# Performance work log

Hardware: AMD Instinct MI355X
Metric: run time of the kernel (lower is better)

The kernel has to match this reference:

```python
import jax, jax.numpy as jnp
import numpy as np

B, S, D = 4, 2048, 1024
H, HD = 16, 64            # num heads, head dim (H*HD == D)
FF = 4096                  # llama intermediate size
EPS = 1e-6
THETA = 10000.0


def rms_norm(x, w):
    v = jnp.mean(jnp.square(x), axis=-1, keepdims=True)
    return x * jax.lax.rsqrt(v + EPS) * w


def apply_rope(x, pos):
    # x: [B,H,S,HD]; HF llama rotate_half convention
    inv = 1.0 / (THETA ** (jnp.arange(0, HD, 2, dtype=jnp.float32) / HD))  # [HD/2]
    ang = pos[:, None].astype(jnp.float32) * inv[None, :]                   # [S,HD/2]
    cos = jnp.concatenate([jnp.cos(ang), jnp.cos(ang)], -1)[None, None]     # [1,1,S,HD]
    sin = jnp.concatenate([jnp.sin(ang), jnp.sin(ang)], -1)[None, None]
    x1, x2 = jnp.split(x, 2, axis=-1)
    return x * cos + jnp.concatenate([-x2, x1], axis=-1) * sin


def setup_inputs() -> dict:
    key = jax.random.key(0)
    ks = jax.random.split(key, 12)
    p = lambda k, shp: (0.02 * jax.random.normal(k, shp, dtype=jnp.float32))
    return {
        "chunk_hidden_states": jax.random.normal(ks[0], (B, S, D), dtype=jnp.float32),
        "Wq": p(ks[1], (D, D)),
        "Wk": p(ks[2], (D, D)),
        "Wv": p(ks[3], (D, D)),
        "Wo": p(ks[4], (D, D)),
        "ln1_w": jnp.ones((D,), dtype=jnp.float32),
        "ln2_w": jnp.ones((D,), dtype=jnp.float32),
        "Wgate": p(ks[5], (FF, D)),
        "Wup": p(ks[6], (FF, D)),
        "Wdown": p(ks[7], (D, FF)),
        "W_out": p(ks[8], (1024, D)),
        "b_out": jnp.zeros((1024,), dtype=jnp.float32),
    }


def reference(chunk_hidden_states, Wq, Wk, Wv, Wo, ln1_w, ln2_w,
              Wgate, Wup, Wdown, W_out, b_out):
    x = chunk_hidden_states                      # [B,S,D]
    pos = jnp.arange(S)

    # --- self attention block ---
    h = rms_norm(x, ln1_w)
    q = (h @ Wq.T).reshape(B, S, H, HD).transpose(0, 2, 1, 3)  # [B,H,S,HD]
    k = (h @ Wk.T).reshape(B, S, H, HD).transpose(0, 2, 1, 3)
    v = (h @ Wv.T).reshape(B, S, H, HD).transpose(0, 2, 1, 3)
    q = apply_rope(q, pos)
    k = apply_rope(k, pos)
    # attention_mask is None when the layer is called directly -> full (non-causal) attention
    scores = jnp.einsum("bhqd,bhkd->bhqk", q, k) / jnp.sqrt(jnp.float32(HD))
    attn = jax.nn.softmax(scores, axis=-1)
    ctx = jnp.einsum("bhqk,bhkd->bhqd", attn, v)             # [B,H,S,HD]
    ctx = ctx.transpose(0, 2, 1, 3).reshape(B, S, D)
    x = x + ctx @ Wo.T

    # --- MLP block (SwiGLU) ---
    h2 = rms_norm(x, ln2_w)
    mlp = (jax.nn.silu(h2 @ Wgate.T) * (h2 @ Wup.T)) @ Wdown.T
    x = x + mlp

    # --- output head ---
    logits = x @ W_out.T + b_out                 # [B,S,1024]
    return logits.reshape(-1, 8, 1024)
```

## Files before the change

### kernel.cpp

```cpp
#include <hip/hip_runtime.h>

#define TB 4
#define TS 2048
#define TD 1024
#define TH 16
#define THD 64
#define TFF 4096
#define TTOK (TB*TS)

typedef unsigned int  uint32;
typedef unsigned short u16;
typedef short s8v __attribute__((ext_vector_type(8)));
typedef short s4bf __attribute__((ext_vector_type(4)));
typedef float f4v __attribute__((ext_vector_type(4)));

#define BF16_MAGIC 0x3f803f80u

__device__ __forceinline__ u16 f2bf(float f){
    uint32 u = __float_as_uint(f);
    u += 0x7fffu + ((u >> 16) & 1u);
    return (u16)(u >> 16);
}
__device__ __forceinline__ float bf2f(u16 h){
    return __uint_as_float(((uint32)h) << 16);
}
__device__ __forceinline__ void gload_lds16(const void* g, void* l){
    __builtin_amdgcn_global_load_lds(
        (const __attribute__((address_space(1))) unsigned int*)g,
        (__attribute__((address_space(3))) unsigned int*)l,
        16, 0, 0);
}
__device__ __forceinline__ void bar(){
    asm volatile("" ::: "memory");
    __builtin_amdgcn_s_barrier();
    asm volatile("" ::: "memory");
}
#define WAITVM(N) asm volatile("s_waitcnt vmcnt(" #N ")" ::: "memory")

struct CvtDesc { const void* src; void* dst; int n; int mode; };
struct CvtArgs { CvtDesc d[13]; };

__global__ __launch_bounds__(256)
void cvt_all(CvtArgs a, const uint32* __restrict__ flag){
    const bool isbf = (*flag == BF16_MAGIC);
    CvtDesc dd = a.d[blockIdx.y];
    if (dd.mode == 2){
        float* cosT = (float*)dd.dst;
        float* sinT = cosT + TS*32;
        for (int i = blockIdx.x*256 + threadIdx.x; i < dd.n; i += 256*gridDim.x){
            int s = i >> 5, f = i & 31;
            double inv = pow(10000.0, -(double)f/32.0);
            double ang = (double)s * inv;
            cosT[i] = (float)cos(ang);
            sinT[i] = (float)sin(ang);
        }
        return;
    }
    int n4 = dd.n >> 2;
    if (dd.mode == 1){
        float* dst = (float*)dd.dst;
        for (int i = blockIdx.x*256 + threadIdx.x; i < n4; i += 256*gridDim.x){
            float4 v;
            if (isbf){
                ushort4 u = ((const ushort4*)dd.src)[i];
                v = make_float4(bf2f(u.x), bf2f(u.y), bf2f(u.z), bf2f(u.w));
            } else v = ((const float4*)dd.src)[i];
            ((float4*)dst)[i] = v;
        }
        return;
    }
    for (int i = blockIdx.x*256 + threadIdx.x; i < n4; i += 256*gridDim.x){
        ushort4 o;
        if (isbf) o = ((const ushort4*)dd.src)[i];
        else {
            float4 v = ((const float4*)dd.src)[i];
            o.x=f2bf(v.x); o.y=f2bf(v.y); o.z=f2bf(v.z); o.w=f2bf(v.w);
        }
        size_t di = i;
        if (dd.mode >= 3){
            int row = i >> 8, c4 = i & 255;
            int drow = ((row >> 6) << 7) + (row & 63) + ((dd.mode == 4) ? 64 : 0);
            di = (size_t)drow*256 + c4;
        }
        ((ushort4*)dd.dst)[di] = o;
    }
}

__global__ __launch_bounds__(256)
void rmsnorm_k(const float* __restrict__ x, const float* __restrict__ w, u16* __restrict__ out){
    int row = blockIdx.x, tid = threadIdx.x;
    float4 xv = ((const float4*)(x + (size_t)row*TD))[tid];
    float s = xv.x*xv.x + xv.y*xv.y + xv.z*xv.z + xv.w*xv.w;
    #pragma unroll
    for (int off = 32; off > 0; off >>= 1) s += __shfl_xor(s, off);
    __shared__ float red[4];
    if ((tid & 63) == 0) red[tid >> 6] = s;
    __syncthreads();
    float tot = red[0]+red[1]+red[2]+red[3];
    float rs = rsqrtf(tot * (1.0f/TD) + 1e-6f);
    float4 wv = ((const float4*)w)[tid];
    ushort4 o;
    o.x = f2bf(xv.x*rs*wv.x); o.y = f2bf(xv.y*rs*wv.y);
    o.z = f2bf(xv.z*rs*wv.z); o.w = f2bf(xv.w*rs*wv.w);
    ((ushort4*)(out + (size_t)row*TD))[tid] = o;
}

enum { EPI_ADDF32 = 1, EPI_OUT = 3, EPI_QKVROPE = 4, EPI_ADDBF16 = 5, EPI_GATEUP = 6 };

template<int EPI>
__global__ __launch_bounds__(256)
void gemm_bt(const u16* __restrict__ A, int lda,
             const u16* __restrict__ W, int ldw,
             int K,
             void* __restrict__ outp, int ldo,
             const float* __restrict__ bias,
             const uint32* __restrict__ flag,
             u16* __restrict__ q_out, u16* __restrict__ k_out, u16* __restrict__ vt_out,
             const float* __restrict__ cosT, const float* __restrict__ sinT,
             const float* __restrict__ resid)
{
    __shared__ __align__(16) u16 SMEM[2*128*64];
    u16* As = SMEM;
    u16* Bs = SMEM + 128*64;
    const int tid  = threadIdx.x;
    const int wave = tid >> 6;
    const int lane = tid & 63;
    const int nbx = gridDim.x;
    const int lin = blockIdx.y * nbx + blockIdx.x;
    const int swz = (lin & 7) * ((nbx * gridDim.y) >> 3) + (lin >> 3);
    const int tm = (swz / nbx) * 128;
    const int tn = (swz % nbx) * 128;
    const int wm = (wave >> 1) * 64;
    const int wn = (wave &  1) * 64;

    f4v acc[4][4] = {};

    const int srow8 = lane >> 3;
    const int ch    = lane & 7;
    const int lrow  = lane & 15;
    const int lq    = lane >> 4;

    const u16* Ag = A + (size_t)(tm + wave*32 + srow8)*lda + ((ch ^ srow8) << 3);
    const u16* Wg = W + (size_t)(tn + wave*32 + srow8)*ldw + ((ch ^ srow8) << 3);

    for (int k0 = 0; k0 < K; k0 += 64){
        __syncthreads();
        #pragma unroll
        for (int i8 = 0; i8 < 4; i8++){
            gload_lds16(Ag + (size_t)(i8*8)*lda + k0, As + (wave*32 + i8*8)*64);
            gload_lds16(Wg + (size_t)(i8*8)*ldw + k0, Bs + (wave*32 + i8*8)*64);
        }
        __syncthreads();

        #pragma unroll
        for (int kk = 0; kk < 2; kk++){
            s8v a[4], b[4];
            #pragma unroll
            for (int i = 0; i < 4; i++){
                int row = wm + i*16 + lrow;
                a[i] = *(const s8v*)(As + row*64 + (((kk*4 + lq) ^ (lrow & 7)) << 3));
            }
            #pragma unroll
            for (int j = 0; j < 4; j++){
                int row = wn + j*16 + lrow;
                b[j] = *(const s8v*)(Bs + row*64 + (((kk*4 + lq) ^ (lrow & 7)) << 3));
            }
            #pragma unroll
            for (int i = 0; i < 4; i++)
                #pragma unroll
                for (int j = 0; j < 4; j++)
                    acc[i][j] = __builtin_amdgcn_mfma_f32_16x16x32_bf16(a[i], b[j], acc[i][j], 0, 0, 0);
        }
    }

    if constexpr (EPI == EPI_QKVROPE){
        const int ncol0 = tn + wn;
        if (ncol0 < 2048){
            u16* dst = (ncol0 < 1024) ? q_out : k_out;
            const int cbase = ncol0 & 1023;
            #pragma unroll
            for (int i = 0; i < 4; i++){
                #pragma unroll
                for (int r = 0; r < 4; r++){
                    int row = tm + wm + i*16 + lq*4 + r;
                    int s = row & (TS-1);
                    #pragma unroll
                    for (int j = 0; j < 2; j++){
                        int d = j*16 + lrow;
                        float c  = cosT[s*32 + d];
                        float sn = sinT[s*32 + d];
                        float x1 = acc[i][j][r], x2 = acc[i][j+2][r];
                        dst[(size_t)row*TD + cbase + d]      = f2bf(x1*c - x2*sn);
                        dst[(size_t)row*TD + cbase + d + 32] = f2bf(x2*c + x1*sn);
                    }
                }
            }
        } else {
            #pragma unroll
            for (int i = 0; i < 4; i++)
                #pragma unroll
                for (int j = 0; j < 4; j++)
                    #pragma unroll
                    for (int r = 0; r < 4; r++){
                        int row = tm + wm + i*16 + lq*4 + r;
                        int col = ncol0 - 2048 + j*16 + lrow;
                        int bb = row >> 11, s = row & (TS-1);
                        int hh = col >> 6, hd = col & 63;
                        vt_out[((size_t)(bb*TH + hh)*THD + hd)*TS + s] = f2bf(acc[i][j][r]);
                    }
        }
        return;
    }

    bool obf = false;
    if (EPI == EPI_OUT) obf = (*flag == BF16_MAGIC);
    #pragma unroll
    for (int i = 0; i < 4; i++){
        #pragma unroll
        for (int j = 0; j < 4; j++){
            #pragma unroll
            for (int r = 0; r < 4; r++){
                int row = tm + wm + i*16 + lq*4 + r;
                int col = tn + wn + j*16 + lrow;
                size_t idx = (size_t)row*ldo + col;
                float val = acc[i][j][r];
                if constexpr (EPI == EPI_ADDF32){
                    float* o = (float*)outp;
                    o[idx] += val;
                } else if constexpr (EPI == EPI_ADDBF16){
                    ((u16*)outp)[idx] = f2bf(resid[idx] + val);
                } else {
                    float v2 = val + bias[col];
                    if (obf) ((u16*)outp)[idx] = f2bf(v2);
                    else     ((float*)outp)[idx] = v2;
                }
            }
        }
    }
}

template<int EPI>
__global__ __launch_bounds__(512, 2)
void gemm256(const u16* __restrict__ A, int lda,
             const u16* __restrict__ W, int ldw,
             int K,
             void* __restrict__ outp, int ldo,
             const float* __restrict__ resid)
{
    __shared__ __align__(16) u16 SM[2][2*256*64];
    const int tid  = threadIdx.x;
    const int wave = tid >> 6;
    const int lane = tid & 63;
    const int wm = wave >> 2;
    const int wn = wave & 3;
    const int lrow = lane & 15;
    const int lq   = lane >> 4;
    const int srow8 = lane >> 3;
    const int ch    = lane & 7;

    const int nbx = gridDim.x;
    const int lin = blockIdx.y * nbx + blockIdx.x;
    const int swz = (lin & 7) * ((nbx * gridDim.y) >> 3) + (lin >> 3);
    const int tm = (swz / nbx) * 256;
    const int tn = (swz % nbx) * 256;

    const int NT = K >> 6;

    const u16* Ag = A + (size_t)(tm + wave*8 + srow8)*lda + ((ch ^ srow8) << 3);
    const u16* Wg = W + (size_t)(tn + wave*8 + srow8)*ldw + ((ch ^ srow8) << 3);

    f4v acc[2][4][2][2] = {};
    s8v a[2][4];
    s8v b[2][2][2];

    auto stageA = [&](int bufi, int g, int t){
        size_t k0 = (size_t)t * 64;
        #pragma unroll
        for (int r = 0; r < 2; r++)
            gload_lds16(Ag + (size_t)(g*128 + r*64)*lda + k0,
                        &SM[bufi][(g*128 + r*64 + wave*8)*64]);
    };
    auto stageB = [&](int bufi, int h, int t){
        size_t k0 = (size_t)t * 64;
        #pragma unroll
        for (int r = 0; r < 2; r++)
            gload_lds16(Wg + (size_t)(h*128 + r*64)*ldw + k0,
                        &SM[bufi][256*64 + (h*128 + r*64 + wave*8)*64]);
    };
    auto ldA = [&](int bufi, int g){
        #pragma unroll
        for (int kk = 0; kk < 2; kk++)
            #pragma unroll
            for (int i = 0; i < 4; i++){
                int row = g*128 + wm*64 + i*16 + lrow;
                a[kk][i] = *(const s8v*)(&SM[bufi][row*64 + (((kk*4 + lq) ^ (lrow & 7)) << 3)]);
            }
    };
    auto ldB = [&](int bufi, int h){
        #pragma unroll
        for (int kk = 0; kk < 2; kk++)
            #pragma unroll
            for (int j = 0; j < 2; j++){
                int row = h*128 + wn*32 + j*16 + lrow;
                b[h][kk][j] = *(const s8v*)(&SM[bufi][256*64 + row*64 + (((kk*4 + lq) ^ (lrow & 7)) << 3)]);
            }
    };
    auto mmac = [&](int g, int h){
        __builtin_amdgcn_s_setprio(1);
        #pragma unroll
        for (int kk = 0; kk < 2; kk++)
            #pragma unroll
            for (int i = 0; i < 4; i++)
                #pragma unroll
                for (int j = 0; j < 2; j++)
                    acc[g][i][h][j] = __builtin_amdgcn_mfma_f32_16x16x32_bf16(
                        a[kk][i], b[h][kk][j], acc[g][i][h][j], 0, 0, 0);
        __builtin_amdgcn_s_setprio(0);
    };

    stageA(0,0,0); stageB(0,0,0); stageB(0,1,0); stageA(0,1,0);
    stageA(1,0,1); stageB(1,0,1); stageB(1,1,1);
    WAITVM(6); bar();

    for (int t = 0; t < NT-2; t += 2){
        ldA(0,0); ldB(0,0);
        stageA(1,1,t+1);
        bar(); mmac(0,0); bar();
        ldB(0,1);
        stageA(0,0,t+2);
        bar(); mmac(0,1); bar();
        ldA(0,1);
        stageB(0,0,t+2);
        bar(); mmac(1,0); bar();
        stageB(0,1,t+2);
        WAITVM(6);
        bar(); mmac(1,1); bar();
        ldA(1,0); ldB(1,0);
        stageA(0,1,t+2);
        bar(); mmac(0,0); bar();
        ldB(1,1);
        stageA(1,0,t+3);
        bar(); mmac(0,1); bar();
        ldA(1,1);
        stageB(1,0,t+3);
        bar(); mmac(1,0); bar();
        stageB(1,1,t+3);
        WAITVM(6);
        bar(); mmac(1,1); bar();
    }
    {
        ldA(0,0); ldB(0,0);
        stageA(1,1,NT-1);
        bar(); mmac(0,0); bar();
        ldB(0,1);
        bar(); mmac(0,1); bar();
        ldA(0,1);
        bar(); mmac(1,0); bar();
        WAITVM(0);
        bar(); mmac(1,1); bar();
        ldA(1,0); ldB(1,0);
        bar(); mmac(0,0); bar();
        ldB(1,1);
        bar(); mmac(0,1); bar();
        ldA(1,1);
        bar(); mmac(1,0); bar();
        mmac(1,1);
    }

    if constexpr (EPI == EPI_GATEUP){
        bar();
        float* X = (float*)&SM[0][0];
        const int uw = wm*2 + (wn & 1);
        if (wn >= 2){
            #pragma unroll
            for (int g = 0; g < 2; g++)
            #pragma unroll
            for (int i = 0; i < 4; i++)
            #pragma unroll
            for (int h = 0; h < 2; h++)
            #pragma unroll
            for (int j = 0; j < 2; j++)
            #pragma unroll
            for (int r = 0; r < 4; r++)
                X[uw*8192 + (g*64 + i*16 + lq*4 + r)*64
                          + ((h*32 + j*16 + lrow) ^ (lq << 3))] = acc[g][i][h][j][r];
        }
        bar();
        if (wn < 2){
            u16* o = (u16*)outp;
            #pragma unroll
            for (int g = 0; g < 2; g++)
            #pragma unroll
            for (int i = 0; i < 4; i++)
            #pragma unroll
            for (int h = 0; h < 2; h++)
            #pragma unroll
            for (int j = 0; j < 2; j++)
            #pragma unroll
            for (int r = 0; r < 4; r++){
                float gv = acc[g][i][h][j][r];
                float uv = X[uw*8192 + (g*64 + i*16 + lq*4 + r)*64
                                     + ((h*32 + j*16 + lrow) ^ (lq << 3))];
                float mres = (gv / (1.0f + __expf(-gv))) * uv;
                int row = tm + g*128 + wm*64 + i*16 + lq*4 + r;
                int ff  = (tn >> 1) + h*64 + wn*32 + j*16 + lrow;
                o[(size_t)row*TFF + ff] = f2bf(mres);
            }
        }
        return;
    }

    if constexpr (EPI == EPI_ADDBF16){
        u16* o = (u16*)outp;
        #pragma unroll
        for (int g = 0; g < 2; g++)
        #pragma unroll
        for (int i = 0; i < 4; i++)
        #pragma unroll
        for (int h = 0; h < 2; h++)
        #pragma unroll
        for (int j = 0; j < 2; j++)
        #pragma unroll
        for (int r = 0; r < 4; r++){
            int row = tm + g*128 + wm*64 + i*16 + lq*4 + r;
            int col = tn + h*128 + wn*32 + j*16 + lrow;
            size_t idx = (size_t)row*ldo + col;
            o[idx] = f2bf(resid[idx] + acc[g][i][h][j][r]);
        }
        return;
    }
}

__global__ __launch_bounds__(256, 2)
void flash_attn_mfma(const u16* __restrict__ qg, const u16* __restrict__ kg,
                     const u16* __restrict__ vt, u16* __restrict__ ctx)
{
    __shared__ u16 Qs[128*64];
    __shared__ u16 Ks[64*64];
    __shared__ u16 VT2[8*64*8];
    const int tid  = threadIdx.x;
    const int wave = tid >> 6;
    const int lane = tid & 63;
    const int qd   = lane >> 4;
    const int mm   = lane & 15;
    const int lin = blockIdx.y * 16 + blockIdx.x;
    const int swz = (lin & 7) * 128 + (lin >> 3);
    const int b  = swz >> 8, h = (swz >> 4) & 15;
    const int q0 = (swz & 15) * 128;
    const size_t tok0 = (size_t)b * TS;
    const u16* vtb = vt + (size_t)(b*TH + h)*THD*TS;
    const int rl = lane >> 3, ch = lane & 7;

    #pragma unroll
    for (int i = 0; i < 4; i++){
        int row = wave*32 + i*8 + rl;
        const u16* gp = qg + (tok0 + q0 + row)*TD + h*THD + ((ch ^ (row & 7)) << 3);
        gload_lds16(gp, Qs + (wave*32 + i*8)*64);
    }
    __syncthreads();

    s8v qf[2][2];
    #pragma unroll
    for (int ct = 0; ct < 2; ct++){
        int row = wave*32 + ct*16 + mm;
        #pragma unroll
        for (int hs = 0; hs < 2; hs++)
            qf[ct][hs] = *(const s8v*)(Qs + row*64 + (((hs*4 + qd) ^ (row & 7)) << 3));
    }

    f4v acc[2][4] = {};
    float mrun[2] = {-3.0e38f, -3.0e38f};
    float lrun[2] = {0.0f, 0.0f};
    const float SC2 = 0.18033688011112042f;

    for (int kt = 0; kt < TS/64; kt++){
        __syncthreads();
        #pragma unroll
        for (int i = 0; i < 2; i++){
            int row = wave*16 + i*8 + rl;
            const u16* gp = kg + (tok0 + kt*64 + row)*TD + h*THD + ((ch ^ (row & 7)) << 3);
            gload_lds16(gp, Ks + (wave*16 + i*8)*64);
        }
        #pragma unroll
        for (int ii = 0; ii < 2; ii++){
            int kb = wave*2 + ii;
            const u16* gp = vtb + (size_t)lane*TS + kt*64 + kb*8;
            gload_lds16(gp, VT2 + kb*64*8);
        }
        __syncthreads();

        f4v sc[4][2] = {};
        #pragma unroll
        for (int rt = 0; rt < 4; rt++){
            int row = rt*16 + mm;
            #pragma unroll
            for (int hs = 0; hs < 2; hs++){
                s8v kf = *(const s8v*)(Ks + row*64 + (((hs*4 + qd) ^ (row & 7)) << 3));
                #pragma unroll
                for (int ct = 0; ct < 2; ct++)
                    sc[rt][ct] = __builtin_amdgcn_mfma_f32_16x16x32_bf16(kf, qf[ct][hs], sc[rt][ct], 0, 0, 0);
            }
        }
        union VU { s4bf h[2]; s8v v; };
        VU vf8[2][4];
        #pragma unroll
        for (int t = 0; t < 2; t++){
            int kbA = 4*t + (qd >> 1);
            #pragma unroll
            for (int n = 0; n < 4; n++){
                const u16* base = VT2 + ((16*n + mm)*8) + ((qd & 1) * 4);
                vf8[t][n].h[0] = *(const s4bf*)(base + kbA*512);
                vf8[t][n].h[1] = *(const s4bf*)(base + (kbA+2)*512);
            }
        }

        #pragma unroll
        for (int ct = 0; ct < 2; ct++){
            float mx = sc[0][ct][0];
            #pragma unroll
            for (int rt = 0; rt < 4; rt++)
                #pragma unroll
                for (int r = 0; r < 4; r++)
                    mx = fmaxf(mx, sc[rt][ct][r]);
            mx = fmaxf(mx, __shfl_xor(mx, 16));
            mx = fmaxf(mx, __shfl_xor(mx, 32));
            float mn = fmaxf(mrun[ct], mx * SC2);
            float alpha = __builtin_amdgcn_exp2f(mrun[ct] - mn);
            mrun[ct] = mn;
            float ls = 0.0f;
            uint32 pk[4][2];
            #pragma unroll
            for (int rt = 0; rt < 4; rt++){
                float p0 = __builtin_amdgcn_exp2f(fmaf(sc[rt][ct][0], SC2, -mn));
                float p1 = __builtin_amdgcn_exp2f(fmaf(sc[rt][ct][1], SC2, -mn));
                float p2 = __builtin_amdgcn_exp2f(fmaf(sc[rt][ct][2], SC2, -mn));
                float p3 = __builtin_amdgcn_exp2f(fmaf(sc[rt][ct][3], SC2, -mn));
                ls += (p0 + p1) + (p2 + p3);
                pk[rt][0] = (__float_as_uint(p0) >> 16) | (__float_as_uint(p1) & 0xFFFF0000u);
                pk[rt][1] = (__float_as_uint(p2) >> 16) | (__float_as_uint(p3) & 0xFFFF0000u);
            }
            ls += __shfl_xor(ls, 16);
            ls += __shfl_xor(ls, 32);
            lrun[ct] = lrun[ct]*alpha + ls;
            #pragma unroll
            for (int r = 0; r < 4; r++){
                float ar = __shfl(alpha, (lane & 48) + qd*4 + r);
                #pragma unroll
                for (int n = 0; n < 4; n++)
                    acc[ct][n][r] *= ar;
            }
            #pragma unroll
            for (int t = 0; t < 2; t++){
                union { uint32 u[4]; s8v s; } pu;
                pu.u[0] = pk[2*t][0];   pu.u[1] = pk[2*t][1];
                pu.u[2] = pk[2*t+1][0]; pu.u[3] = pk[2*t+1][1];
                #pragma unroll
                for (int n = 0; n < 4; n++)
                    acc[ct][n] = __builtin_amdgcn_mfma_f32_16x16x32_bf16(pu.s, vf8[t][n].v, acc[ct][n], 0, 0, 0);
            }
        }
    }
    #pragma unroll
    for (int ct = 0; ct < 2; ct++){
        float rli = 1.0f / lrun[ct];
        #pragma unroll
        for (int r = 0; r < 4; r++){
            float ir = __shfl(rli, (lane & 48) + qd*4 + r);
            int row = q0 + wave*32 + ct*16 + qd*4 + r;
            u16* op = ctx + (tok0 + row)*TD + h*THD + mm;
            #pragma unroll
            for (int n = 0; n < 4; n++)
                op[16*n] = f2bf(acc[ct][n][r] * ir);
        }
    }
}

extern "C" void kernel_launch(void* const* d_in, const int* in_sizes, int n_in,
                              void* d_out, int out_size, void* d_ws, size_t ws_size,
                              hipStream_t stream)
{
    const uint32* flag = (const uint32*)d_in[5];
    char* ws = (char*)d_ws;
    size_t off = 0;
    auto alloc = [&](size_t bytes) -> void* {
        void* p = ws + off;
        off += (bytes + 255) & ~(size_t)255;
        return p;
    };
    float* xf   = (float*)alloc((size_t)TTOK*TD*4);
    u16*   hbf  = (u16*)  alloc((size_t)TTOK*TD*2);
    u16*   qb   = (u16*)  alloc((size_t)TTOK*TD*2);
    u16*   kb   = (u16*)  alloc((size_t)TTOK*TD*2);
    u16*   cb   = (u16*)  alloc((size_t)TTOK*TD*2);
    u16*   vt   = (u16*)  alloc((size_t)TTOK*TD*2);
    u16*   wqkv = (u16*)  alloc((size_t)3*TD*TD*2);
    u16*   wo   = (u16*)  alloc((size_t)TD*TD*2);
    u16*   wfu  = (u16*)  alloc((size_t)2*TFF*TD*2);
    u16*   wd   = (u16*)  alloc((size_t)TD*TFF*2);
    u16*   wou  = (u16*)  alloc((size_t)TD*TD*2);
    float* ln1  = (float*)alloc(TD*4);
    float* ln2  = (float*)alloc(TD*4);
    float* bo   = (float*)alloc(TD*4);
    float* cosT = (float*)alloc((size_t)TS*32*4*2);
    float* sinT = cosT + TS*32;
    u16*   mbuf = qb;
    (void)ws_size; (void)in_sizes; (void)n_in; (void)out_size;

    CvtArgs ca;
    ca.d[0]  = { d_in[0],  xf,            TTOK*TD, 1 };
    ca.d[1]  = { d_in[1],  wqkv,          TD*TD,   0 };
    ca.d[2]  = { d_in[2],  wqkv + (size_t)TD*TD,   TD*TD, 0 };
    ca.d[3]  = { d_in[3],  wqkv + (size_t)2*TD*TD, TD*TD, 0 };
    ca.d[4]  = { d_in[4],  wo,            TD*TD,   0 };
    ca.d[5]  = { d_in[7],  wfu,           TFF*TD,  3 };
    ca.d[6]  = { d_in[8],  wfu,           TFF*TD,  4 };
    ca.d[7]  = { d_in[9],  wd,            TD*TFF,  0 };
    ca.d[8]  = { d_in[10], wou,           TD*TD,   0 };
    ca.d[9]  = { d_in[5],  ln1,           TD,      1 };
    ca.d[10] = { d_in[6],  ln2,           TD,      1 };
    ca.d[11] = { d_in[11], bo,            TD,      1 };
    ca.d[12] = { nullptr,  cosT,          TS*32,   2 };
    cvt_all<<<dim3(256,13),256,0,stream>>>(ca, flag);

    rmsnorm_k<<<TTOK,256,0,stream>>>(xf, ln1, hbf);
    gemm_bt<EPI_QKVROPE><<<dim3(24, TTOK/128),256,0,stream>>>(
        hbf, TD, wqkv, TD, TD, nullptr, 0, nullptr, nullptr,
        qb, kb, vt, cosT, sinT, nullptr);
    flash_attn_mfma<<<dim3(TS/128, TB*TH),256,0,stream>>>(qb, kb, vt, cb);
    gemm_bt<EPI_ADDF32><<<dim3(TD/128, TTOK/128),256,0,stream>>>(
        cb, TD, wo, TD, TD, xf, TD, nullptr, nullptr,
        nullptr, nullptr, nullptr, nullptr, nullptr, nullptr);

    rmsnorm_k<<<TTOK,256,0,stream>>>(xf, ln2, hbf);
    gemm256<EPI_GATEUP><<<dim3(2*TFF/256, TTOK/256),512,0,stream>>>(
        hbf, TD, wfu, TD, TD, mbuf, TFF, nullptr);
    gemm_bt<EPI_ADDBF16><<<dim3(TD/128, TTOK/128),256,0,stream>>>(
        mbuf, TFF, wd, TFF, TFF, hbf, TD, nullptr, nullptr,
        nullptr, nullptr, nullptr, nullptr, nullptr, xf);

    gemm_bt<EPI_OUT><<<dim3(TD/128, TTOK/128),256,0,stream>>>(
        hbf, TD, wou, TD, TD, d_out, TD, bo, flag,
        nullptr, nullptr, nullptr, nullptr, nullptr, nullptr);
}
```

Baseline: 702.6 us.

## Shrink B fragment registers and reorder GEMM quadrant schedule with per-iteration buffers

The GEMM main loop now keeps a single B fragment set instead of one per half-tile. It walks the four 128x128 quadrants in a snake order (00, 01, 11, 10) so B is reloaded from LDS when needed. The loop is rolled to one K-tile per iteration with buffer index t&1, and the staging order of global-to-LDS copies is reshuffled. The aim is to cut VGPR pressure, possibly raising occupancy or freeing registers, at the cost of extra LDS reads for B and a different overlap pattern between copies and MFMAs.

After: 676.6 us. -3.7%, faster.

```diff
diff --git a/kernel.cpp b/kernel.cpp
--- a/kernel.cpp
+++ b/kernel.cpp
@@ -271,7 +271,7 @@
 
     f4v acc[2][4][2][2] = {};
     s8v a[2][4];
-    s8v b[2][2][2];
+    s8v b[2][2];
 
     auto stageA = [&](int bufi, int g, int t){
         size_t k0 = (size_t)t * 64;
@@ -302,7 +302,7 @@
             #pragma unroll
             for (int j = 0; j < 2; j++){
                 int row = h*128 + wn*32 + j*16 + lrow;
-                b[h][kk][j] = *(const s8v*)(&SM[bufi][256*64 + row*64 + (((kk*4 + lq) ^ (lrow & 7)) << 3)]);
+                b[kk][j] = *(const s8v*)(&SM[bufi][256*64 + row*64 + (((kk*4 + lq) ^ (lrow & 7)) << 3)]);
             }
     };
     auto mmac = [&](int g, int h){
@@ -314,57 +314,53 @@
                 #pragma unroll
                 for (int j = 0; j < 2; j++)
                     acc[g][i][h][j] = __builtin_amdgcn_mfma_f32_16x16x32_bf16(
-                        a[kk][i], b[h][kk][j], acc[g][i][h][j], 0, 0, 0);
+                        a[kk][i], b[kk][j], acc[g][i][h][j], 0, 0, 0);
         __builtin_amdgcn_s_setprio(0);
     };
 
     stageA(0,0,0); stageB(0,0,0); stageB(0,1,0); stageA(0,1,0);
-    stageA(1,0,1); stageB(1,0,1); stageB(1,1,1);
+    stageA(1,0,1); stageB(1,1,1); stageA(1,1,1);
     WAITVM(6); bar();
 
-    for (int t = 0; t < NT-2; t += 2){
-        ldA(0,0); ldB(0,0);
-        stageA(1,1,t+1);
+    for (int t = 0; t < NT-2; t++){
+        const int buf = t & 1, nb = buf ^ 1;
+        ldA(buf,0); ldB(buf,0);
+        stageB(nb,0,t+1);
         bar(); mmac(0,0); bar();
-        ldB(0,1);
-        stageA(0,0,t+2);
+        ldB(buf,1);
+        stageA(buf,0,t+2);
         bar(); mmac(0,1); bar();
-        ldA(0,1);
-        stageB(0,0,t+2);
+        ldA(buf,1);
+        stageB(buf,1,t+2);
+        bar(); mmac(1,1); bar();
+        ldB(buf,0);
+        stageA(buf,1,t+2);
+        WAITVM(6);
         bar(); mmac(1,0); bar();
-        stageB(0,1,t+2);
-        WAITVM(6);
+    }
+    {
+        const int buf = (NT-2) & 1, nb = buf ^ 1;
+        ldA(buf,0); ldB(buf,0);
+        stageB(nb,0,NT-1);
+        bar(); mmac(0,0); bar();
+        ldB(buf,1);
+        bar(); mmac(0,1); bar();
+        ldA(buf,1);
         bar(); mmac(1,1); bar();
-        ldA(1,0); ldB(1,0);
-        stageA(0,1,t+2);
+        ldB(buf,0);
+        WAITVM(0);
+        bar(); mmac(1,0); bar();
+    }
+    {
+        const int buf = (NT-1) & 1;
+        ldA(buf,0); ldB(buf,0);
         bar(); mmac(0,0); bar();
-        ldB(1,1);
-        stageA(1,0,t+3);
+        ldB(buf,1);
         bar(); mmac(0,1); bar();
-        ldA(1,1);
-        stageB(1,0,t+3);
+        ldA(buf,1);
+        bar(); mmac(1,1); bar();
+        ldB(buf,0);
         bar(); mmac(1,0); bar();
-        stageB(1,1,t+3);
-        WAITVM(6);
-        bar(); mmac(1,1); bar();
-    }
-    {
-        ldA(0,0); ldB(0,0);
-        stageA(1,1,NT-1);
-        bar(); mmac(0,0); bar();
-        ldB(0,1);
-        bar(); mmac(0,1); bar();
-        ldA(0,1);
-        bar(); mmac(1,0); bar();
-        WAITVM(0);
-        bar(); mmac(1,1); bar();
-        ldA(1,0); ldB(1,0);
-        bar(); mmac(0,0); bar();
-        ldB(1,1);
-        bar(); mmac(0,1); bar();
-        ldA(1,1);
-        bar(); mmac(1,0); bar();
-        mmac(1,1);
     }
 
     if constexpr (EPI == EPI_GATEUP){
```
